# Performance work log

Measured on AMD Instinct MI355X. Metric: run time of the kernel, lower is better.

## Reference

```python
import jax, jax.numpy as jnp
import numpy as np

N, E, L, D = 4, 64, 512, 768


def setup_inputs() -> dict:
    key = jax.random.key(0)
    k1, k2, k3, k4 = jax.random.split(key, 4)
    doc_state = jax.random.normal(k1, (N, L, D), dtype=jnp.float32)
    # 0/1 entity membership mask, float as in the torch module's multiply
    entity_mapping = jax.random.randint(k2, (N, E, L), 0, 2).astype(jnp.float32)
    # lens consistent with the mask; clamp to >=1 to avoid divide-by-zero
    entity_lens = jnp.maximum(entity_mapping.sum(axis=-1), 1.0)
    W = jax.random.normal(k3, (D, 2 * D), dtype=jnp.float32) * 0.02  # torch Linear weight [out, in]
    b = jnp.zeros((D,), dtype=jnp.float32)
    return {"doc_state": doc_state, "entity_mapping": entity_mapping,
            "entity_lens": entity_lens, "W": W, "b": b}


def reference(doc_state, entity_mapping, entity_lens, W, b):
    # entity_states: N x E x L x d (the large broadcast intermediate)
    entity_states = entity_mapping[:, :, :, None] * doc_state[:, None, :, :]
    max_pooled = jnp.max(entity_states, axis=2)                      # N x E x d
    mean_pooled = jnp.sum(entity_states, axis=2) / entity_lens[:, :, None]  # N x E x d
    output = jnp.concatenate([max_pooled, mean_pooled], axis=2)      # N x E x 2d
    return jnp.einsum('nek,dk->ned', output, W) + b                  # N x E x d
```

## Files before the change

### kernel.cpp

```cpp
#include <hip/hip_runtime.h>
#include <hip/hip_bf16.h>
#include <math.h>

#define PN 4
#define PE 64
#define PL 512
#define PD 768
#define PK2 (2 * PD)
#define PM (PN * PE)

#define EG 4
#define DCW 256
#define NPOOLB 192
#define NCVT2 144
#define NXCD 8

using bf16x8 = __attribute__((ext_vector_type(8))) short;
using f32x4  = __attribute__((ext_vector_type(4))) float;

static __device__ __forceinline__ unsigned short f2bf(float x) {
    unsigned int u = __float_as_uint(x);
    unsigned int r = (u + 0x7FFFu + ((u >> 16) & 1u)) >> 16;
    return (unsigned short)r;
}

__global__ __launch_bounds__(1024) void pool_v10(
    const float* __restrict__ doc,
    const float* __restrict__ map,
    const float* __restrict__ lens,
    const float* __restrict__ W,
    unsigned short* __restrict__ Pb,
    unsigned short* __restrict__ Wb)
{
    const int bid = blockIdx.x;
    const int tid = threadIdx.x;

    if (bid >= NPOOLB) {
        const size_t i = ((size_t)(bid - NPOOLB) * 1024 + tid) * 8;
        const float4 a = *reinterpret_cast<const float4*>(W + i);
        const float4 c = *reinterpret_cast<const float4*>(W + i + 4);
        union { unsigned short s[8]; uint4 v; } r;
        r.s[0] = f2bf(a.x); r.s[1] = f2bf(a.y); r.s[2] = f2bf(a.z); r.s[3] = f2bf(a.w);
        r.s[4] = f2bf(c.x); r.s[5] = f2bf(c.y); r.s[6] = f2bf(c.z); r.s[7] = f2bf(c.w);
        *reinterpret_cast<uint4*>(Wb + i) = r.v;
        return;
    }

    __shared__ float lbuf[16][EG][DCW];

    const int xcd = bid & (NXCD - 1);
    const int idx = bid >> 3;
    const int n   = xcd >> 1;
    const int eg  = (xcd & 1) * 8 + idx / 3;
    const int dc  = idx % 3;
    const int e0  = eg * EG;
    const int d0  = dc * DCW;
    const int w    = tid >> 6;
    const int lane = tid & 63;

    unsigned int mk[EG];
    #pragma unroll
    for (int e = 0; e < EG; ++e) {
        const float m = map[((size_t)n * PE + e0 + e) * PL + w * 32 + (lane & 31)];
        mk[e] = (unsigned int)__ballot(m != 0.0f);
    }

    const float* docp = doc + ((size_t)n * PL + w * 32) * PD + d0 + lane * 4;

    float4 mx[EG], sm[EG];
    #pragma unroll
    for (int e = 0; e < EG; ++e) {
        mx[e] = make_float4(-INFINITY, -INFINITY, -INFINITY, -INFINITY);
        sm[e] = make_float4(0.f, 0.f, 0.f, 0.f);
    }

    #pragma unroll 8
    for (int l = 0; l < 32; ++l) {
        const float4 v = *reinterpret_cast<const float4*>(docp + (size_t)l * PD);
        #pragma unroll
        for (int e = 0; e < EG; ++e) {
            const float mval = ((mk[e] >> l) & 1u) ? 1.0f : 0.0f;
            const float cx = mval * v.x, cy = mval * v.y;
            const float cz = mval * v.z, cw = mval * v.w;
            sm[e].x += cx; sm[e].y += cy; sm[e].z += cz; sm[e].w += cw;
            mx[e].x = fmaxf(mx[e].x, cx); mx[e].y = fmaxf(mx[e].y, cy);
            mx[e].z = fmaxf(mx[e].z, cz); mx[e].w = fmaxf(mx[e].w, cw);
        }
    }

    #pragma unroll
    for (int e = 0; e < EG; ++e)
        *reinterpret_cast<float4*>(&lbuf[w][e][lane * 4]) = mx[e];
    __syncthreads();
    {
        const int e = tid >> 8;
        const int d = tid & 255;
        float m = lbuf[0][e][d];
        #pragma unroll
        for (int ww = 1; ww < 16; ++ww) m = fmaxf(m, lbuf[ww][e][d]);
        const int ne = n * PE + e0 + e;
        Pb[(size_t)ne * PK2 + d0 + d] = f2bf(m);
    }
    __syncthreads();

    #pragma unroll
    for (int e = 0; e < EG; ++e)
        *reinterpret_cast<float4*>(&lbuf[w][e][lane * 4]) = sm[e];
    __syncthreads();
    {
        const int e = tid >> 8;
        const int d = tid & 255;
        float s = lbuf[0][e][d];
        #pragma unroll
        for (int ww = 1; ww < 16; ++ww) s += lbuf[ww][e][d];
        const int ne = n * PE + e0 + e;
        Pb[(size_t)ne * PK2 + PD + d0 + d] = f2bf(s * (1.0f / lens[ne]));
    }
}

__global__ __launch_bounds__(128) void gemm_ks2x(
    const unsigned short* __restrict__ Pb,
    const unsigned short* __restrict__ Wb,
    const float* __restrict__ b,
    float* __restrict__ out)
{
    __shared__ f32x4 red[64];

    const int w    = threadIdx.x >> 6;
    const int lane = threadIdx.x & 63;
    const int bid  = blockIdx.x;
    const int xcd  = bid & (NXCD - 1);
    const int idx  = bid >> 3;
    const int ct = xcd * 6 + (idx >> 4);
    const int rt = idx & 15;
    const int r0 = rt * 16, d0 = ct * 16;

    const int fr = lane & 15;
    const int kg = lane >> 4;
    const int kb = w * (PK2 / 2);

    const unsigned short* pA = Pb + (size_t)(r0 + fr) * PK2 + kb + kg * 8;
    const unsigned short* pB = Wb + (size_t)(d0 + fr) * PK2 + kb + kg * 8;

    f32x4 acc0 = {0.f, 0.f, 0.f, 0.f};
    f32x4 acc1 = {0.f, 0.f, 0.f, 0.f};
    #pragma unroll
    for (int k0 = 0; k0 < PK2 / 2; k0 += 64) {
        const bf16x8 a0 = *reinterpret_cast<const bf16x8*>(pA + k0);
        const bf16x8 b0 = *reinterpret_cast<const bf16x8*>(pB + k0);
        acc0 = __builtin_amdgcn_mfma_f32_16x16x32_bf16(a0, b0, acc0, 0, 0, 0);
        const bf16x8 a1 = *reinterpret_cast<const bf16x8*>(pA + k0 + 32);
        const bf16x8 b1 = *reinterpret_cast<const bf16x8*>(pB + k0 + 32);
        acc1 = __builtin_amdgcn_mfma_f32_16x16x32_bf16(a1, b1, acc1, 0, 0, 0);
    }
    f32x4 acc = acc0 + acc1;

    if (w == 1) red[lane] = acc;
    __syncthreads();
    if (w == 0) {
        acc += red[lane];
        const int c = d0 + fr;
        const float bias = b[c];
        #pragma unroll
        for (int j = 0; j < 4; ++j)
            out[(size_t)(r0 + kg * 4 + j) * PD + c] = acc[j] + bias;
    }
}

__global__ __launch_bounds__(256) void fused_kernel(
    const float* __restrict__ doc, const float* __restrict__ map,
    const float* __restrict__ lens, const float* __restrict__ W,
    const float* __restrict__ b, float* __restrict__ out)
{
    __shared__ float Prow[PK2];
    const int ne = blockIdx.x, n = ne >> 6, t = threadIdx.x;
    const float* docn = doc + (size_t)n * PL * PD;
    const float* mrow = map + (size_t)ne * PL;
    float mx0=-INFINITY, mx1=-INFINITY, mx2=-INFINITY, s0=0.f, s1=0.f, s2=0.f;
    bool has_zero = false;
    for (int l = 0; l < PL; ++l) {
        const float m = mrow[l];
        if (m != 0.0f) {
            const float* dr = docn + (size_t)l * PD;
            const float a = dr[t], c = dr[t+256], e = dr[t+512];
            mx0=fmaxf(mx0,a); s0+=a; mx1=fmaxf(mx1,c); s1+=c; mx2=fmaxf(mx2,e); s2+=e;
        } else has_zero = true;
    }
    if (has_zero) { mx0=fmaxf(mx0,0.f); mx1=fmaxf(mx1,0.f); mx2=fmaxf(mx2,0.f); }
    const float invlen = 1.0f / lens[ne];
    Prow[t]=mx0; Prow[t+256]=mx1; Prow[t+512]=mx2;
    Prow[PD+t]=s0*invlen; Prow[PD+t+256]=s1*invlen; Prow[PD+t+512]=s2*invlen;
    __syncthreads();
    #pragma unroll
    for (int i = 0; i < 3; ++i) {
        const int d = t + i*256;
        const float* wrow = W + (size_t)d * PK2;
        float acc = 0.f;
        for (int k = 0; k < PK2; k += 4) {
            const float4 w = *reinterpret_cast<const float4*>(&wrow[k]);
            acc += Prow[k]*w.x + Prow[k+1]*w.y + Prow[k+2]*w.z + Prow[k+3]*w.w;
        }
        out[(size_t)ne * PD + d] = acc + b[d];
    }
}

extern "C" void kernel_launch(void* const* d_in, const int* in_sizes, int n_in,
                              void* d_out, int out_size, void* d_ws, size_t ws_size,
                              hipStream_t stream) {
    const float* doc  = (const float*)d_in[0];
    const float* map  = (const float*)d_in[1];
    const float* lens = (const float*)d_in[2];
    const float* W    = (const float*)d_in[3];
    const float* b    = (const float*)d_in[4];
    float* out = (float*)d_out;

    const size_t pb_bytes = (size_t)PM * PK2 * sizeof(unsigned short);
    const size_t wb_bytes = (size_t)PD * PK2 * sizeof(unsigned short);
    const size_t need     = pb_bytes + wb_bytes;

    if (ws_size >= need) {
        unsigned short* Pb = (unsigned short*)d_ws;
        unsigned short* Wb = (unsigned short*)((char*)d_ws + pb_bytes);
        pool_v10<<<dim3(NPOOLB + NCVT2), dim3(1024), 0, stream>>>(
            doc, map, lens, W, Pb, Wb);
        gemm_ks2x<<<dim3((PM / 16) * (PD / 16)), dim3(128), 0, stream>>>(Pb, Wb, b, out);
    } else {
        fused_kernel<<<dim3(PM), dim3(256), 0, stream>>>(doc, map, lens, W, b, out);
    }
}
```

Measured before the change: 26.64 us.

## Halve entities per pool block and reduce max and sum concurrently

Each pooling block now handles 2 entities instead of 4, doubling the pool grid to 384 blocks so more of the GPU is busy and each thread holds fewer accumulator registers. The shared-memory reduction now writes max and sum partials into separate buffers at once, and the two halves of the block reduce them in parallel, removing one reduction phase and two barriers. The cost is that each doc tile is loaded twice as often across blocks, which raises L2 and HBM read traffic.

```diff
diff --git a/kernel.cpp b/kernel.cpp
--- a/kernel.cpp
+++ b/kernel.cpp
@@ -9,9 +9,9 @@
 #define PK2 (2 * PD)
 #define PM (PN * PE)
 
-#define EG 4
+#define EG 2
 #define DCW 256
-#define NPOOLB 192
+#define NPOOLB 384
 #define NCVT2 144
 #define NXCD 8
 
@@ -24,7 +24,7 @@
     return (unsigned short)r;
 }
 
-__global__ __launch_bounds__(1024) void pool_v10(
+__global__ __launch_bounds__(1024) void pool_v12(
     const float* __restrict__ doc,
     const float* __restrict__ map,
     const float* __restrict__ lens,
@@ -46,12 +46,13 @@
         return;
     }
 
-    __shared__ float lbuf[16][EG][DCW];
+    __shared__ float lmax[16][EG][DCW];
+    __shared__ float lsum[16][EG][DCW];
 
     const int xcd = bid & (NXCD - 1);
     const int idx = bid >> 3;
     const int n   = xcd >> 1;
-    const int eg  = (xcd & 1) * 8 + idx / 3;
+    const int eg  = (xcd & 1) * 16 + idx / 3;
     const int dc  = idx % 3;
     const int e0  = eg * EG;
     const int d0  = dc * DCW;
@@ -89,31 +90,25 @@
     }
 
     #pragma unroll
-    for (int e = 0; e < EG; ++e)
-        *reinterpret_cast<float4*>(&lbuf[w][e][lane * 4]) = mx[e];
+    for (int e = 0; e < EG; ++e) {
+        *reinterpret_cast<float4*>(&lmax[w][e][lane * 4]) = mx[e];
+        *reinterpret_cast<float4*>(&lsum[w][e][lane * 4]) = sm[e];
+    }
     __syncthreads();
-    {
-        const int e = tid >> 8;
-        const int d = tid & 255;
-        float m = lbuf[0][e][d];
-        #pragma unroll
-        for (int ww = 1; ww < 16; ++ww) m = fmaxf(m, lbuf[ww][e][d]);
-        const int ne = n * PE + e0 + e;
+
+    const int slot = tid & 511;
+    const int e = slot >> 8;
+    const int d = slot & 255;
+    const int ne = n * PE + e0 + e;
+    if (tid < 512) {
+        float m = lmax[0][e][d];
+        #pragma unroll
+        for (int ww = 1; ww < 16; ++ww) m = fmaxf(m, lmax[ww][e][d]);
         Pb[(size_t)ne * PK2 + d0 + d] = f2bf(m);
-    }
-    __syncthreads();
-
-    #pragma unroll
-    for (int e = 0; e < EG; ++e)
-        *reinterpret_cast<float4*>(&lbuf[w][e][lane * 4]) = sm[e];
-    __syncthreads();
-    {
-        const int e = tid >> 8;
-        const int d = tid & 255;
-        float s = lbuf[0][e][d];
-        #pragma unroll
-        for (int ww = 1; ww < 16; ++ww) s += lbuf[ww][e][d];
-        const int ne = n * PE + e0 + e;
+    } else {
+        float s = lsum[0][e][d];
+        #pragma unroll
+        for (int ww = 1; ww < 16; ++ww) s += lsum[ww][e][d];
         Pb[(size_t)ne * PK2 + PD + d0 + d] = f2bf(s * (1.0f / lens[ne]));
     }
 }
@@ -221,7 +216,7 @@
     if (ws_size >= need) {
         unsigned short* Pb = (unsigned short*)d_ws;
         unsigned short* Wb = (unsigned short*)((char*)d_ws + pb_bytes);
-        pool_v10<<<dim3(NPOOLB + NCVT2), dim3(1024), 0, stream>>>(
+        pool_v12<<<dim3(NPOOLB + NCVT2), dim3(1024), 0, stream>>>(
             doc, map, lens, W, Pb, Wb);
         gemm_ks2x<<<dim3((PM / 16) * (PD / 16)), dim3(128), 0, stream>>>(Pb, Wb, b, out);
     } else {
```

Result: slower. 27.32 us (+2.5%).
